# Performance work log

Measured on AMD Instinct MI355X. Metric: run time of the kernel, lower is better.

Reference implementation:

```python
import jax, jax.numpy as jnp
import numpy as np

EPS = 1e-06

def _mlp(x, Ws):
    # chained Linear(bias=False) + ReLU, applied per depth layer
    for i in range(Ws.shape[0]):
        x = jax.nn.relu(x @ Ws[i].T)  # torch Linear: x @ W^T
    return x

def setup_inputs() -> dict:
    key = jax.random.key(0)
    k1, k2, k3 = jax.random.split(key, 3)
    B, N, D, depth = 4, 4096, 64, 2
    x = jax.random.normal(k1, (B, N, D), dtype=jnp.float32)
    # kaiming-uniform-ish init scale for Linear(64,64)
    s = 1.0 / np.sqrt(D)
    W_enc = jax.random.uniform(k2, (depth, D, D), dtype=jnp.float32, minval=-s, maxval=s)
    W_dec = jax.random.uniform(k3, (depth, D, D), dtype=jnp.float32, minval=-s, maxval=s)
    return {"x": x, "W_enc": W_enc, "W_dec": W_dec}

def reference(x, W_enc, W_dec):
    y = _mlp(x, W_enc)                                   # [B,N,D]
    y = y / (jnp.linalg.norm(y, axis=-1, keepdims=True) + EPS)
    cmp_matrix = jnp.einsum('bnd,bmd->bnm', y, y)        # [B,N,N] (no softmax)
    y = jnp.einsum('bnm,bmd->bnd', cmp_matrix, y)        # [B,N,D]
    return _mlp(y, W_dec)
```

## Files before the change

### kernel.cpp

```cpp
#include <hip/hip_runtime.h>


typedef _Float16 h8 __attribute__((ext_vector_type(8)));
typedef float    f4 __attribute__((ext_vector_type(4)));
typedef unsigned long long u64;

constexpr unsigned KEY = 0xC5E3A1D7u;

#define RFL(v) __builtin_amdgcn_readfirstlane(v)

__device__ __forceinline__ void ic_store(float* p, float v) {
    __hip_atomic_store(p, v, __ATOMIC_RELAXED, __HIP_MEMORY_SCOPE_AGENT);
}
__device__ __forceinline__ u64 ic_load64(const u64* p) {
    return __hip_atomic_load(p, __ATOMIC_RELAXED, __HIP_MEMORY_SCOPE_AGENT);
}
__device__ __forceinline__ void ic_store64(u64* p, u64 v) {
    __hip_atomic_store(p, v, __ATOMIC_RELAXED, __HIP_MEMORY_SCOPE_AGENT);
}
__device__ __forceinline__ void ic_store_u(unsigned* p, unsigned v) {
    __hip_atomic_store(p, v, __ATOMIC_RELAXED, __HIP_MEMORY_SCOPE_AGENT);
}
__device__ __forceinline__ unsigned ic_load_u(const unsigned* p) {
    return __hip_atomic_load(p, __ATOMIC_RELAXED, __HIP_MEMORY_SCOPE_AGENT);
}

__device__ __forceinline__ f4 mfma16(h8 a, h8 b, f4 c) {
    return __builtin_amdgcn_mfma_f32_16x16x32_f16(a, b, c, 0, 0, 0);
}
__device__ __forceinline__ h8 mkfrag_f32(const float* p) {
    const float4 a = *(const float4*)p;
    const float4 b = *(const float4*)(p + 4);
    h8 r;
    r[0]=(_Float16)a.x; r[1]=(_Float16)a.y; r[2]=(_Float16)a.z; r[3]=(_Float16)a.w;
    r[4]=(_Float16)b.x; r[5]=(_Float16)b.y; r[6]=(_Float16)b.z; r[7]=(_Float16)b.w;
    return r;
}

union F2U { float f[2]; u64 v; };

__global__ __launch_bounds__(512) void fused(
        const float* __restrict__ x,
        const float* __restrict__ We,
        const float* __restrict__ Wd,
        float* __restrict__ out,
        float* __restrict__ partG,
        u64* __restrict__ Gu,
        unsigned* __restrict__ flagP,
        unsigned* __restrict__ flagG) {
    __shared__ __align__(16) float sT [32][68];
    __shared__ __align__(16) float sTt[64][36];
    __shared__ __align__(16) float sGf[64][68];
    __shared__ __align__(16) float sSS[32][4];
    __shared__ float sScale[32];

    const int t = threadIdx.x;
    const int l = t & 63, c = l & 15, g = l >> 4;
    const int w = RFL(t >> 6), ti = w >> 2, tj = w & 3;
    const int blk = blockIdx.x, bb = blk >> 7;
    const long base  = (long)blk * 2048;
    const long baseG = (long)blk * 4096;

    h8 wE0[2], wE1[2], wD0[2], wD1[2];
#pragma unroll
    for (int kh = 0; kh < 2; ++kh) {
        const int n = tj * 16 + c;
        wE0[kh] = mkfrag_f32(We +        n * 64 + kh * 32 + g * 8);
        wE1[kh] = mkfrag_f32(We + 4096 + n * 64 + kh * 32 + g * 8);
        wD0[kh] = mkfrag_f32(Wd +        n * 64 + kh * 32 + g * 8);
        wD1[kh] = mkfrag_f32(Wd + 4096 + n * 64 + kh * 32 + g * 8);
    }

    {
        const float4 v = ((const float4*)(x + base))[t];
        *(float4*)&sT[t >> 4][(t & 15) * 4] = v;
    }
    __syncthreads();

    auto rowfragT = [&](int row, int kh) -> h8 {
        return mkfrag_f32(&sT[row][kh * 32 + g * 8]);
    };

    f4 d = {0.f, 0.f, 0.f, 0.f};
#pragma unroll
    for (int kh = 0; kh < 2; ++kh) d = mfma16(rowfragT(16*ti + c, kh), wE0[kh], d);
    __syncthreads();
#pragma unroll
    for (int i = 0; i < 4; ++i) sT[16*ti + 4*g + i][16*tj + c] = fmaxf(d[i], 0.f);
    __syncthreads();

    d = (f4){0.f, 0.f, 0.f, 0.f};
#pragma unroll
    for (int kh = 0; kh < 2; ++kh) d = mfma16(rowfragT(16*ti + c, kh), wE1[kh], d);
    float hv[4];
#pragma unroll
    for (int i = 0; i < 4; ++i) hv[i] = fmaxf(d[i], 0.f);

    float sq[4];
#pragma unroll
    for (int i = 0; i < 4; ++i) sq[i] = hv[i] * hv[i];
#pragma unroll
    for (int m = 1; m < 16; m <<= 1) {
#pragma unroll
        for (int i = 0; i < 4; ++i) sq[i] += __shfl_xor(sq[i], m);
    }
    if (c == 0) {
#pragma unroll
        for (int i = 0; i < 4; ++i) sSS[16*ti + 4*g + i][tj] = sq[i];
    }
    __syncthreads();
    if (t < 32) {
        const float4 s4 = *(const float4*)&sSS[t][0];
        sScale[t] = 1.f / (sqrtf(s4.x + s4.y + s4.z + s4.w) + 1e-6f);
    }
    __syncthreads();

    {
        float yv4[4];
#pragma unroll
        for (int i = 0; i < 4; ++i) {
            const int row = 16*ti + 4*g + i;
            yv4[i] = hv[i] * sScale[row];
            sT[row][16*tj + c] = yv4[i];
        }
        *(float4*)&sTt[16*tj + c][16*ti + 4*g] =
            make_float4(yv4[0], yv4[1], yv4[2], yv4[3]);
    }
    __syncthreads();

    {
        const h8 fB  = mkfrag_f32(&sTt[16*tj + c][g * 8]);
        const h8 fA0 = mkfrag_f32(&sTt[16*ti + c][g * 8]);
        const h8 fA1 = mkfrag_f32(&sTt[16*(ti + 2) + c][g * 8]);
        const f4 z4 = {0.f, 0.f, 0.f, 0.f};
        const f4 ga0 = mfma16(fA0, fB, z4);
        const f4 ga1 = mfma16(fA1, fB, z4);
#pragma unroll
        for (int i = 0; i < 4; ++i) {
            ic_store(&partG[baseG + (16*ti       + 4*g + i) * 64 + 16*tj + c], ga0[i]);
            ic_store(&partG[baseG + (16*(ti + 2) + 4*g + i) * 64 + 16*tj + c], ga1[i]);
        }
    }

    asm volatile("s_waitcnt vmcnt(0)" ::: "memory");
    __syncthreads();
    if (t == 0) ic_store_u(&flagP[blk], KEY);

    if (blk < 64) {
        const int rb = blk >> 4, s = blk & 15;
        if (t < 128) {
            unsigned spins = 0;
            while (ic_load_u(&flagP[rb * 128 + t]) != KEY) {
                __builtin_amdgcn_s_sleep(1);
                if (++spins > 30000000u) break;
            }
        }
        __syncthreads();
        if (t < 128) {
            const u64* src = (const u64*)partG + (long)rb * 128 * 2048 + s * 128 + t;
            float a0 = 0.f, a1 = 0.f;
#pragma unroll 16
            for (int j = 0; j < 128; ++j) {
                F2U p; p.v = ic_load64(src + (long)j * 2048);
                a0 += p.f[0]; a1 += p.f[1];
            }
            F2U o; o.f[0] = a0; o.f[1] = a1;
            ic_store64(&Gu[rb * 2048 + s * 128 + t], o.v);
            asm volatile("s_waitcnt vmcnt(0)" ::: "memory");
        }
        __syncthreads();
        if (t == 0) ic_store_u(&flagG[rb * 16 + s], KEY);
    }

    if (t < 16) {
        unsigned spins = 0;
        while (ic_load_u(&flagG[bb * 16 + t]) != KEY) {
            __builtin_amdgcn_s_sleep(1);
            if (++spins > 30000000u) break;
        }
    }
    __syncthreads();
    asm volatile("" ::: "memory");

    {
#pragma unroll
        for (int kk = 0; kk < 4; ++kk) {
            const int u = kk * 512 + t;
            F2U p; p.v = ic_load64(&Gu[bb * 2048 + u]);
            const int e = u * 2;
            sGf[e >> 6][e & 63]       = p.f[0];
            sGf[e >> 6][(e & 63) + 1] = p.f[1];
        }
    }
    __syncthreads();

    f4 z = {0.f, 0.f, 0.f, 0.f};
#pragma unroll
    for (int kh = 0; kh < 2; ++kh)
        z = mfma16(rowfragT(16*ti + c, kh),
                   mkfrag_f32(&sGf[16*tj + c][kh * 32 + g * 8]), z);
    __syncthreads();
#pragma unroll
    for (int i = 0; i < 4; ++i) sT[16*ti + 4*g + i][16*tj + c] = z[i];
    __syncthreads();

    d = (f4){0.f, 0.f, 0.f, 0.f};
#pragma unroll
    for (int kh = 0; kh < 2; ++kh) d = mfma16(rowfragT(16*ti + c, kh), wD0[kh], d);
    __syncthreads();
#pragma unroll
    for (int i = 0; i < 4; ++i) sT[16*ti + 4*g + i][16*tj + c] = fmaxf(d[i], 0.f);
    __syncthreads();

    d = (f4){0.f, 0.f, 0.f, 0.f};
#pragma unroll
    for (int kh = 0; kh < 2; ++kh) d = mfma16(rowfragT(16*ti + c, kh), wD1[kh], d);
#pragma unroll
    for (int i = 0; i < 4; ++i)
        out[base + (16*ti + 4*g + i) * 64 + 16*tj + c] = fmaxf(d[i], 0.f);
}

extern "C" void kernel_launch(void* const* d_in, const int* in_sizes, int n_in,
                              void* d_out, int out_size, void* d_ws, size_t ws_size,
                              hipStream_t stream) {
    const float* x  = (const float*)d_in[0];
    const float* We = (const float*)d_in[1];
    const float* Wd = (const float*)d_in[2];
    float* outp = (float*)d_out;
    char*  ws   = (char*)d_ws;

    float*    partG = (float*)ws;
    u64*      Gu    = (u64*)(ws + (8u << 20));
    unsigned* flagP = (unsigned*)(Gu + 4 * 2048);
    unsigned* flagG = flagP + 512;

    fused<<<512, 512, 0, stream>>>(x, We, Wd, outp, partG, Gu, flagP, flagG);
}
```

Baseline: 25.86 us.

## Store partial Gram matrices in fp16 fragment order and parallelize reduction

Per-block partial Gram matrices are now packed as fp16 in MFMA fragment layout and written with 64-bit stores, halving the global traffic of the partial and reduced Gram exchange. The cross-block reduction uses 256 threads split into four chunks combined through shared memory instead of 128 threads each looping over all 128 blocks. Consumers unpack the fragment layout back into the shared Gram tile. This adds fp16 rounding of partial and summed Gram entries, which may lose accuracy or overflow for large sums, and adds a shared-memory reduction step. The flag key changes so stale flags from earlier runs do not match.

```diff
diff --git a/kernel.cpp b/kernel.cpp
--- a/kernel.cpp
+++ b/kernel.cpp
@@ -5,13 +5,10 @@
 typedef float    f4 __attribute__((ext_vector_type(4)));
 typedef unsigned long long u64;
 
-constexpr unsigned KEY = 0xC5E3A1D7u;
+constexpr unsigned KEY = 0xD7A5C3F1u;
 
 #define RFL(v) __builtin_amdgcn_readfirstlane(v)
 
-__device__ __forceinline__ void ic_store(float* p, float v) {
-    __hip_atomic_store(p, v, __ATOMIC_RELAXED, __HIP_MEMORY_SCOPE_AGENT);
-}
 __device__ __forceinline__ u64 ic_load64(const u64* p) {
     return __hip_atomic_load(p, __ATOMIC_RELAXED, __HIP_MEMORY_SCOPE_AGENT);
 }
@@ -37,20 +34,22 @@
     return r;
 }
 
-union F2U { float f[2]; u64 v; };
+union HU { _Float16 h; unsigned short u; };
+union PK { u64 v; unsigned short u[4]; };
 
 __global__ __launch_bounds__(512) void fused(
         const float* __restrict__ x,
         const float* __restrict__ We,
         const float* __restrict__ Wd,
         float* __restrict__ out,
-        float* __restrict__ partG,
+        u64* __restrict__ partGu,
         u64* __restrict__ Gu,
         unsigned* __restrict__ flagP,
         unsigned* __restrict__ flagG) {
     __shared__ __align__(16) float sT [32][68];
     __shared__ __align__(16) float sTt[64][36];
     __shared__ __align__(16) float sGf[64][68];
+    __shared__ __align__(16) float4 sRed[64][4];
     __shared__ __align__(16) float sSS[32][4];
     __shared__ float sScale[32];
 
@@ -58,8 +57,7 @@
     const int l = t & 63, c = l & 15, g = l >> 4;
     const int w = RFL(t >> 6), ti = w >> 2, tj = w & 3;
     const int blk = blockIdx.x, bb = blk >> 7;
-    const long base  = (long)blk * 2048;
-    const long baseG = (long)blk * 4096;
+    const long base = (long)blk * 2048;
 
     h8 wE0[2], wE1[2], wD0[2], wD1[2];
 #pragma unroll
@@ -135,11 +133,14 @@
         const f4 z4 = {0.f, 0.f, 0.f, 0.f};
         const f4 ga0 = mfma16(fA0, fB, z4);
         const f4 ga1 = mfma16(fA1, fB, z4);
+        PK o0, o1;
 #pragma unroll
         for (int i = 0; i < 4; ++i) {
-            ic_store(&partG[baseG + (16*ti       + 4*g + i) * 64 + 16*tj + c], ga0[i]);
-            ic_store(&partG[baseG + (16*(ti + 2) + 4*g + i) * 64 + 16*tj + c], ga1[i]);
-        }
+            HU a; a.h = (_Float16)ga0[i]; o0.u[i] = a.u;
+            HU b; b.h = (_Float16)ga1[i]; o1.u[i] = b.u;
+        }
+        ic_store64(&partGu[(long)blk * 1024 + 2 * t],     o0.v);
+        ic_store64(&partGu[(long)blk * 1024 + 2 * t + 1], o1.v);
     }
 
     asm volatile("s_waitcnt vmcnt(0)" ::: "memory");
@@ -156,16 +157,34 @@
             }
         }
         __syncthreads();
-        if (t < 128) {
-            const u64* src = (const u64*)partG + (long)rb * 128 * 2048 + s * 128 + t;
-            float a0 = 0.f, a1 = 0.f;
+        if (t < 256) {
+            const int slot_l = t & 63, q4 = t >> 6;
+            const u64* src = partGu + (long)rb * 128 * 1024 + s * 64 + slot_l;
+            float a0 = 0.f, a1 = 0.f, a2 = 0.f, a3 = 0.f;
 #pragma unroll 16
-            for (int j = 0; j < 128; ++j) {
-                F2U p; p.v = ic_load64(src + (long)j * 2048);
-                a0 += p.f[0]; a1 += p.f[1];
+            for (int j = q4 * 32; j < q4 * 32 + 32; ++j) {
+                PK p; p.v = ic_load64(src + (long)j * 1024);
+                HU e0, e1, e2, e3;
+                e0.u = p.u[0]; e1.u = p.u[1]; e2.u = p.u[2]; e3.u = p.u[3];
+                a0 += (float)e0.h; a1 += (float)e1.h;
+                a2 += (float)e2.h; a3 += (float)e3.h;
             }
-            F2U o; o.f[0] = a0; o.f[1] = a1;
-            ic_store64(&Gu[rb * 2048 + s * 128 + t], o.v);
+            sRed[slot_l][q4] = make_float4(a0, a1, a2, a3);
+        }
+        __syncthreads();
+        if (t < 64) {
+            const float4 r0 = sRed[t][0], r1 = sRed[t][1];
+            const float4 r2 = sRed[t][2], r3 = sRed[t][3];
+            const float f0 = ((r0.x + r1.x) + (r2.x + r3.x));
+            const float f1 = ((r0.y + r1.y) + (r2.y + r3.y));
+            const float f2 = ((r0.z + r1.z) + (r2.z + r3.z));
+            const float f3 = ((r0.w + r1.w) + (r2.w + r3.w));
+            PK o;
+            { HU z; z.h = (_Float16)f0; o.u[0] = z.u; }
+            { HU z; z.h = (_Float16)f1; o.u[1] = z.u; }
+            { HU z; z.h = (_Float16)f2; o.u[2] = z.u; }
+            { HU z; z.h = (_Float16)f3; o.u[3] = z.u; }
+            ic_store64(&Gu[rb * 1024 + s * 64 + t], o.v);
             asm volatile("s_waitcnt vmcnt(0)" ::: "memory");
         }
         __syncthreads();
@@ -184,12 +203,19 @@
 
     {
 #pragma unroll
-        for (int kk = 0; kk < 4; ++kk) {
+        for (int kk = 0; kk < 2; ++kk) {
             const int u = kk * 512 + t;
-            F2U p; p.v = ic_load64(&Gu[bb * 2048 + u]);
-            const int e = u * 2;
-            sGf[e >> 6][e & 63]       = p.f[0];
-            sGf[e >> 6][(e & 63) + 1] = p.f[1];
+            PK p; p.v = ic_load64(&Gu[bb * 1024 + u]);
+            const int t_src = u >> 1, pp = u & 1;
+            const int w_s = t_src >> 6, l_s = t_src & 63;
+            const int ti_s = (w_s >> 2) + 2 * pp, tj_s = w_s & 3;
+            const int c_s = l_s & 15, g_s = l_s >> 4;
+            const int col = 16 * tj_s + c_s;
+#pragma unroll
+            for (int i = 0; i < 4; ++i) {
+                HU a; a.u = p.u[i];
+                sGf[16 * ti_s + 4 * g_s + i][col] = (float)a.h;
+            }
         }
     }
     __syncthreads();
@@ -229,10 +255,10 @@
     float* outp = (float*)d_out;
     char*  ws   = (char*)d_ws;
 
-    float*    partG = (float*)ws;
-    u64*      Gu    = (u64*)(ws + (8u << 20));
-    unsigned* flagP = (unsigned*)(Gu + 4 * 2048);
-    unsigned* flagG = flagP + 512;
-
-    fused<<<512, 512, 0, stream>>>(x, We, Wd, outp, partG, Gu, flagP, flagG);
-}
+    u64*      partGu = (u64*)ws;
+    u64*      Gu     = partGu + 512 * 1024;
+    unsigned* flagP  = (unsigned*)(Gu + 4 * 1024);
+    unsigned* flagG  = flagP + 512;
+
+    fused<<<512, 512, 0, stream>>>(x, We, Wd, outp, partGu, Gu, flagP, flagG);
+}
```

New measurement: 23.73 us. -8.2%, faster.
